# Optimization experiments

Measured on AMD Instinct MI355X. Metric: run time of the kernel, lower is better.

The kernel has to match this reference:

```python
import jax, jax.numpy as jnp
from jax import lax
import numpy as np

NPOINT, RADIUS, NSAMPLE = 1024, 0.2, 32
MLP = [64, 64, 128]
IN_CH = 35  # 3 coord channels + 32 point features
EPS = 1e-5


def farthest_point_sample(xyz, npoint):
    # xyz: (B, N, 3) -> (B, npoint) int32. Deterministic start at index 0.
    B, N, _ = xyz.shape

    def step(carry, _):
        dist, farthest = carry  # (B,N), (B,)
        centroid = jnp.take_along_axis(xyz, farthest[:, None, None], axis=1)  # (B,1,3)
        d = jnp.sum((xyz - centroid) ** 2, axis=-1)  # (B,N)
        dist = jnp.minimum(dist, d)
        nxt = jnp.argmax(dist, axis=-1).astype(jnp.int32)
        return (dist, nxt), farthest

    init = (jnp.full((B, N), 1e10, xyz.dtype), jnp.zeros((B,), jnp.int32))
    _, idxs = lax.scan(step, init, None, length=npoint)
    return idxs.T  # (B, npoint)


def gather_points(points, idx):
    # points: (B, N, C); idx: (B, ...) int -> (B, ..., C)
    return jax.vmap(lambda p, i: p[i])(points, idx)


def query_ball_point(radius, nsample, xyz, new_xyz):
    # xyz: (B,N,3), new_xyz: (B,S,3) -> (B,S,nsample) int32
    B, N, _ = xyz.shape
    sqrdists = jnp.sum((new_xyz[:, :, None, :] - xyz[:, None, :, :]) ** 2, axis=-1)  # (B,S,N)
    group_idx = jnp.where(sqrdists > radius ** 2, N, jnp.arange(N, dtype=jnp.int32))
    group_idx = jnp.sort(group_idx, axis=-1)[:, :, :nsample]
    first = group_idx[:, :, :1]
    return jnp.where(group_idx == N, first, group_idx)


def sa_forward(xyz, points, params):
    B, N, C = xyz.shape
    fps_idx = farthest_point_sample(xyz, NPOINT)
    new_xyz = gather_points(xyz, fps_idx)  # (B,S,3)
    idx = query_ball_point(RADIUS, NSAMPLE, xyz, new_xyz)  # (B,S,K)
    grouped_xyz = gather_points(xyz, idx)  # (B,S,K,3)
    grouped_xyz_norm = grouped_xyz - new_xyz[:, :, None, :]
    grouped_points = gather_points(points, idx)  # (B,S,K,D)
    new_points = jnp.concatenate([grouped_xyz_norm, grouped_points], axis=-1)  # (B,S,K,Cin)
    x = new_points.transpose(0, 3, 2, 1)  # (B, Cin, K, S)
    for w, b, g, be in params:
        x = jnp.einsum('oi,biks->boks', w, x) + b[None, :, None, None]  # 1x1 conv
        mean = x.mean(axis=(0, 2, 3), keepdims=True)  # BatchNorm2d, training mode
        var = x.var(axis=(0, 2, 3), keepdims=True)
        x = (x - mean) / jnp.sqrt(var + EPS)
        x = jax.nn.relu(g[None, :, None, None] * x + be[None, :, None, None])
    new_points_out = x.max(axis=2)  # max over nsample -> (B, Cout, S)
    return new_xyz, new_points_out


def setup_inputs() -> dict:
    key = jax.random.key(0)
    ks = jax.random.split(key, 16)
    B, N, D = 16, 4096, 32
    inp = {
        'xyz': jax.random.uniform(ks[0], (B, N, 3), dtype=jnp.float32),
        'points': jax.random.normal(ks[1], (B, N, D), dtype=jnp.float32),
    }
    last = IN_CH
    for li, out_ch in enumerate(MLP):
        inp[f'w{li}'] = jax.random.normal(ks[2 + 4 * li], (out_ch, last), dtype=jnp.float32) * 0.05
        inp[f'b{li}'] = jnp.zeros((out_ch,), jnp.float32)
        inp[f'g{li}'] = jnp.ones((out_ch,), jnp.float32)
        inp[f'be{li}'] = jnp.zeros((out_ch,), jnp.float32)
        last = out_ch
    return inp


def reference(xyz, points, w0, b0, g0, be0, w1, b1, g1, be1, w2, b2, g2, be2):
    params = [(w0, b0, g0, be0), (w1, b1, g1, be1), (w2, b2, g2, be2)]
    return sa_forward(xyz, points, params)
```

## Files before the change

kernel.cpp:

```cpp
#include <hip/hip_runtime.h>
#include <stdint.h>

#define BATCH   16
#define NPTS    4096
#define NPOINT  1024
#define NSAMPLE 32
#define NPOS    (BATCH*NPOINT*NSAMPLE)
#define EPSV    1e-5f

typedef unsigned short ushort_t;
typedef unsigned int uint_t;
typedef unsigned long long u64;
typedef __attribute__((ext_vector_type(8))) short bf16x8;
typedef __attribute__((ext_vector_type(4))) float f32x4;

__device__ inline ushort_t f2bf(float f) {
    uint_t u = __float_as_uint(f);
    u += 0x7fffu + ((u >> 16) & 1u);
    return (ushort_t)(u >> 16);
}
__device__ inline void unpack8(uint4 u, float* f) {
    f[0] = __uint_as_float(u.x << 16); f[1] = __uint_as_float(u.x & 0xffff0000u);
    f[2] = __uint_as_float(u.y << 16); f[3] = __uint_as_float(u.y & 0xffff0000u);
    f[4] = __uint_as_float(u.z << 16); f[5] = __uint_as_float(u.z & 0xffff0000u);
    f[6] = __uint_as_float(u.w << 16); f[7] = __uint_as_float(u.w & 0xffff0000u);
}
__device__ inline uint4 pack8(const float* a) {
    uint4 r;
    r.x = (uint_t)f2bf(a[0]) | ((uint_t)f2bf(a[1]) << 16);
    r.y = (uint_t)f2bf(a[2]) | ((uint_t)f2bf(a[3]) << 16);
    r.z = (uint_t)f2bf(a[4]) | ((uint_t)f2bf(a[5]) << 16);
    r.w = (uint_t)f2bf(a[6]) | ((uint_t)f2bf(a[7]) << 16);
    return r;
}

__global__ void zero_kernel(float* __restrict__ p, int n) {
    int i = blockIdx.x * blockDim.x + threadIdx.x;
    if (i < n) p[i] = 0.f;
}

#define DPP_MAX_STAGE(CTRL) do {                                              \
    uint_t _lo2 = __builtin_amdgcn_update_dpp(lo, lo, CTRL, 0xf, 0xf, false); \
    uint_t _hi2 = __builtin_amdgcn_update_dpp(hi, hi, CTRL, 0xf, 0xf, false); \
    u64 _o = ((u64)_hi2 << 32) | _lo2;                                        \
    u64 _v = ((u64)hi << 32) | lo;                                            \
    bool _g = _o > _v;                                                        \
    lo = _g ? _lo2 : lo; hi = _g ? _hi2 : hi;                                 \
} while (0)

__global__ __launch_bounds__(256) void fps_kernel(const float* __restrict__ xyz,
                                                  float* __restrict__ new_xyz) {
    __shared__ float4 lxyz[NPTS];
    __shared__ u64 wbest[2][4];
    __shared__ int fpsidx[NPOINT];
    const int b = blockIdx.x;
    const int tid = threadIdx.x;
    const float* base = xyz + (size_t)b * NPTS * 3;
    for (int n = tid; n < NPTS; n += 256) {
        lxyz[n] = make_float4(base[3 * n], base[3 * n + 1], base[3 * n + 2], 0.f);
    }
    __syncthreads();

    float px[16], py[16], pz[16], dist[16];
    uint_t lowc[16];
#pragma unroll
    for (int j = 0; j < 16; j++) {
        float4 v = lxyz[tid + j * 256];
        px[j] = v.x; py[j] = v.y; pz[j] = v.z;
        dist[j] = 1e10f;
        lowc[j] = ~(uint_t)(tid + j * 256);
    }
    if (tid == 0) fpsidx[0] = 0;
    int cur = 0;
    const int lane = tid & 63, wid = tid >> 6;

    for (int it = 1; it < NPOINT; ++it) {
        float4 c = lxyz[cur];
#pragma unroll
        for (int j = 0; j < 16; j++) {
            float dx = __fsub_rn(px[j], c.x);
            float dy = __fsub_rn(py[j], c.y);
            float dz = __fsub_rn(pz[j], c.z);
            float d = __fadd_rn(__fadd_rn(__fmul_rn(dx, dx), __fmul_rn(dy, dy)),
                                __fmul_rn(dz, dz));
            dist[j] = fminf(dist[j], d);
        }
        u64 t[8];
#pragma unroll
        for (int j = 0; j < 8; j++) {
            u64 a = ((u64)__float_as_uint(dist[j]) << 32) | lowc[j];
            u64 d2 = ((u64)__float_as_uint(dist[j + 8]) << 32) | lowc[j + 8];
            t[j] = a > d2 ? a : d2;
        }
#pragma unroll
        for (int j = 0; j < 4; j++) { u64 o = t[j + 4]; t[j] = t[j] > o ? t[j] : o; }
        t[0] = t[0] > t[1] ? t[0] : t[1];
        t[2] = t[2] > t[3] ? t[2] : t[3];
        u64 v = t[0] > t[2] ? t[0] : t[2];

        uint_t lo = (uint_t)v, hi = (uint_t)(v >> 32);
        DPP_MAX_STAGE(0x111);
        DPP_MAX_STAGE(0x112);
        DPP_MAX_STAGE(0x114);
        DPP_MAX_STAGE(0x118);
        DPP_MAX_STAGE(0x142);
        DPP_MAX_STAGE(0x143);
        uint_t mlo = __builtin_amdgcn_readlane(lo, 63);
        uint_t mhi = __builtin_amdgcn_readlane(hi, 63);

        const int par = it & 1;
        if (lane == 0) wbest[par][wid] = ((u64)mhi << 32) | mlo;
        __syncthreads();
        u64 b0 = wbest[par][0], b1 = wbest[par][1];
        u64 b2 = wbest[par][2], b3 = wbest[par][3];
        u64 m01 = b0 > b1 ? b0 : b1;
        u64 m23 = b2 > b3 ? b2 : b3;
        u64 bb = m01 > m23 ? m01 : m23;
        cur = (int)(~(uint_t)bb) & (NPTS - 1);
        if (tid == 0) fpsidx[it] = cur;
    }
    __syncthreads();
    float* ob = new_xyz + (size_t)b * NPOINT * 3;
    for (int s = tid; s < NPOINT; s += 256) {
        float4 v = lxyz[fpsidx[s]];
        ob[3 * s + 0] = v.x; ob[3 * s + 1] = v.y; ob[3 * s + 2] = v.z;
    }
}

__global__ __launch_bounds__(256) void ballq_kernel(const float* __restrict__ xyz,
                                                    const float* __restrict__ new_xyz,
                                                    int* __restrict__ gidx) {
    const int gw = (int)((blockIdx.x * 256 + threadIdx.x) >> 6);
    const int lane = threadIdx.x & 63;
    const int b = gw / NPOINT, s = gw % NPOINT;
    const float* nb = new_xyz + ((size_t)b * NPOINT + s) * 3;
    const float cx = nb[0], cy = nb[1], cz = nb[2];
    const float* xb = xyz + (size_t)b * NPTS * 3;
    const float r2 = (float)(0.2 * 0.2);
    int cnt = 0;
    int first = -1;
    int* out = gidx + (size_t)gw * NSAMPLE;
    for (int j0 = 0; j0 < NPTS; j0 += 64) {
        int j = j0 + lane;
        float dx = __fsub_rn(xb[j * 3 + 0], cx);
        float dy = __fsub_rn(xb[j * 3 + 1], cy);
        float dz = __fsub_rn(xb[j * 3 + 2], cz);
        float d = __fadd_rn(__fadd_rn(__fmul_rn(dx, dx), __fmul_rn(dy, dy)),
                            __fmul_rn(dz, dz));
        bool pred = !(d > r2);
        u64 mask = __ballot(pred);
        if (first < 0 && mask != 0ull) first = j0 + (__ffsll((long long)mask) - 1);
        int before = __popcll(mask & ((1ull << lane) - 1ull));
        int slot = cnt + before;
        if (pred && slot < NSAMPLE) out[slot] = j;
        cnt += (int)__popcll(mask);
        if (cnt >= NSAMPLE) break;
    }
    if (cnt < NSAMPLE) {
        if (lane >= cnt && lane < NSAMPLE) out[lane] = first;
    }
}

__global__ __launch_bounds__(256) void conv1_mfma(const float* __restrict__ xyz,
                                                  const float* __restrict__ points,
                                                  const float* __restrict__ new_xyz,
                                                  const int* __restrict__ gidx,
                                                  const float* __restrict__ W,
                                                  const float* __restrict__ bias,
                                                  ushort_t* __restrict__ Y) {
    const int lane = threadIdx.x & 63, wid = threadIdx.x >> 6;
    const int l15 = lane & 15, quad = lane >> 4;
    const int p0 = blockIdx.x * 128 + wid * 32;

    bf16x8 Bp[4], Bx[4];
#pragma unroll
    for (int nt = 0; nt < 4; nt++) {
        const float* wr = W + (size_t)(nt * 16 + l15) * 35;
#pragma unroll
        for (int q = 0; q < 8; q++) Bp[nt][q] = (short)f2bf(wr[3 + quad * 8 + q]);
#pragma unroll
        for (int q = 0; q < 8; q++)
            Bx[nt][q] = (quad == 0 && q < 3) ? (short)f2bf(wr[q]) : (short)0;
    }
    f32x4 acc[2][4];
#pragma unroll
    for (int mt = 0; mt < 2; mt++)
#pragma unroll
        for (int nt = 0; nt < 4; nt++) acc[mt][nt] = (f32x4){0.f, 0.f, 0.f, 0.f};

#pragma unroll
    for (int mt = 0; mt < 2; mt++) {
        const int p = p0 + mt * 16 + l15;
        const int b = p >> 15, s = (p & 32767) >> 5;
        const int j = gidx[p];
        const float* pr = points + ((size_t)(b * NPTS + j)) * 32 + quad * 8;
        bf16x8 Ap, Ax;
#pragma unroll
        for (int q = 0; q < 8; q++) Ap[q] = (short)f2bf(pr[q]);
#pragma unroll
        for (int q = 0; q < 8; q++) Ax[q] = 0;
        const float* xp = xyz + ((size_t)(b * NPTS + j)) * 3;
        const float* nz = new_xyz + ((size_t)(b * NPOINT + s)) * 3;
        if (quad == 0) {
            Ax[0] = (short)f2bf(xp[0] - nz[0]);
            Ax[1] = (short)f2bf(xp[1] - nz[1]);
            Ax[2] = (short)f2bf(xp[2] - nz[2]);
        }
#pragma unroll
        for (int nt = 0; nt < 4; nt++) {
            acc[mt][nt] = __builtin_amdgcn_mfma_f32_16x16x32_bf16(Ap, Bp[nt], acc[mt][nt], 0, 0, 0);
            acc[mt][nt] = __builtin_amdgcn_mfma_f32_16x16x32_bf16(Ax, Bx[nt], acc[mt][nt], 0, 0, 0);
        }
    }
#pragma unroll
    for (int nt = 0; nt < 4; nt++) {
        const int ch = nt * 16 + l15;
        const float bs = bias[ch];
#pragma unroll
        for (int mt = 0; mt < 2; mt++) {
            const int pb = p0 + mt * 16 + quad * 4;
#pragma unroll
            for (int r = 0; r < 4; r++)
                Y[(size_t)(pb + r) * 64 + ch] = f2bf(acc[mt][nt][r] + bs);
        }
    }
}

template <int IN, int OUT>
__global__ __launch_bounds__(256) void convN_mfma(const ushort_t* __restrict__ Yin,
                                                  const float* __restrict__ scale,
                                                  const float* __restrict__ shift,
                                                  const float* __restrict__ W,
                                                  const float* __restrict__ bias,
                                                  ushort_t* __restrict__ Yout) {
    constexpr int NT = OUT / 16;
    const int lane = threadIdx.x & 63, wid = threadIdx.x >> 6;
    const int l15 = lane & 15, quad = lane >> 4;
    const int p0 = blockIdx.x * 128 + wid * 32;

    float sc[2][8], sh[2][8];
#pragma unroll
    for (int kq = 0; kq < 2; kq++) {
        const int i0 = kq * 32 + quad * 8;
#pragma unroll
        for (int q = 0; q < 8; q++) { sc[kq][q] = scale[i0 + q]; sh[kq][q] = shift[i0 + q]; }
    }
    bf16x8 Bf[NT][2];
#pragma unroll
    for (int nt = 0; nt < NT; nt++)
#pragma unroll
        for (int kq = 0; kq < 2; kq++) {
            const float* wr = W + (size_t)(nt * 16 + l15) * IN + kq * 32 + quad * 8;
#pragma unroll
            for (int q = 0; q < 8; q++) Bf[nt][kq][q] = (short)f2bf(wr[q]);
        }

    bf16x8 Af[2][2];
#pragma unroll
    for (int mt = 0; mt < 2; mt++)
#pragma unroll
        for (int kq = 0; kq < 2; kq++) {
            const ushort_t* yr = Yin + (size_t)(p0 + mt * 16 + l15) * IN + kq * 32 + quad * 8;
            uint4 u = *(const uint4*)yr;
            float f[8]; unpack8(u, f);
#pragma unroll
            for (int q = 0; q < 8; q++) {
                float x = fmaxf(fmaf(f[q], sc[kq][q], sh[kq][q]), 0.f);
                Af[mt][kq][q] = (short)f2bf(x);
            }
        }

    f32x4 acc[2][NT];
#pragma unroll
    for (int mt = 0; mt < 2; mt++)
#pragma unroll
        for (int nt = 0; nt < NT; nt++) acc[mt][nt] = (f32x4){0.f, 0.f, 0.f, 0.f};
#pragma unroll
    for (int mt = 0; mt < 2; mt++)
#pragma unroll
        for (int nt = 0; nt < NT; nt++) {
            acc[mt][nt] = __builtin_amdgcn_mfma_f32_16x16x32_bf16(Af[mt][0], Bf[nt][0], acc[mt][nt], 0, 0, 0);
            acc[mt][nt] = __builtin_amdgcn_mfma_f32_16x16x32_bf16(Af[mt][1], Bf[nt][1], acc[mt][nt], 0, 0, 0);
        }
#pragma unroll
    for (int nt = 0; nt < NT; nt++) {
        const int ch = nt * 16 + l15;
        const float bs = bias[ch];
#pragma unroll
        for (int mt = 0; mt < 2; mt++) {
            const int pb = p0 + mt * 16 + quad * 4;
#pragma unroll
            for (int r = 0; r < 4; r++)
                Yout[(size_t)(pb + r) * OUT + ch] = f2bf(acc[mt][nt][r] + bs);
        }
    }
}

template <int OUT>
__global__ __launch_bounds__(256) void stats_kernel(const ushort_t* __restrict__ Y,
                                                    float* __restrict__ sums,
                                                    float* __restrict__ sq) {
    constexpr int CH8 = OUT / 8;
    constexpr int ROWS = 256 / CH8;
    constexpr int PPB = ROWS * 32;
    const int oc = threadIdx.x % CH8;
    const int row = threadIdx.x / CH8;
    const int p0 = blockIdx.x * PPB + row;
    float s[8], q[8];
#pragma unroll
    for (int i = 0; i < 8; i++) { s[i] = 0.f; q[i] = 0.f; }
    for (int jj = 0; jj < 32; jj++) {
        int p = p0 + jj * ROWS;
        uint4 u = *(const uint4*)(Y + (size_t)p * OUT + oc * 8);
        float f[8];
        unpack8(u, f);
#pragma unroll
        for (int i = 0; i < 8; i++) { s[i] += f[i]; q[i] += f[i] * f[i]; }
    }
#pragma unroll
    for (int m = CH8; m < 64; m <<= 1) {
#pragma unroll
        for (int i = 0; i < 8; i++) {
            s[i] += __shfl_xor(s[i], m, 64);
            q[i] += __shfl_xor(q[i], m, 64);
        }
    }
    __shared__ float lsq[4][CH8][16];
    const int wid = threadIdx.x >> 6, lane = threadIdx.x & 63;
    if (lane < CH8) {
#pragma unroll
        for (int i = 0; i < 8; i++) {
            lsq[wid][lane][i] = s[i];
            lsq[wid][lane][8 + i] = q[i];
        }
    }
    __syncthreads();
    if (threadIdx.x < OUT) {
        int ch = threadIdx.x;
        int oc2 = ch >> 3, i = ch & 7;
        float ssum = 0.f, qsum = 0.f;
#pragma unroll
        for (int w = 0; w < 4; w++) {
            ssum += lsq[w][oc2][i];
            qsum += lsq[w][oc2][8 + i];
        }
        atomicAdd(sums + ch, ssum);
        atomicAdd(sq + ch, qsum);
    }
}

__global__ void finalize_kernel(const float* __restrict__ sums, const float* __restrict__ sq,
                                const float* __restrict__ g, const float* __restrict__ be,
                                float* __restrict__ scale, float* __restrict__ shift, int OUT) {
    int c = threadIdx.x;
    if (c < OUT) {
        float mean = sums[c] * (1.f / (float)NPOS);
        float var = sq[c] * (1.f / (float)NPOS) - mean * mean;
        float inv = 1.f / sqrtf(var + EPSV);
        float sc = g[c] * inv;
        scale[c] = sc;
        shift[c] = be[c] - mean * sc;
    }
}

__global__ __launch_bounds__(256) void final_kernel(const ushort_t* __restrict__ Y3,
                                                    const float* __restrict__ scale,
                                                    const float* __restrict__ shift,
                                                    float* __restrict__ out) {
    const int b = blockIdx.x >> 5;
    const int stile = (blockIdx.x & 31) * 32;
    const int sl = threadIdx.x >> 3;
    const int oc = threadIdx.x & 7;
    const int s = stile + sl;
    const size_t base = ((size_t)(b * NPOINT + s)) * 32 * 128 + oc * 16;
    float vmax[16];
#pragma unroll
    for (int i = 0; i < 16; i++) vmax[i] = 0.f;
    for (int k = 0; k < 32; k++) {
        const ushort_t* yp = Y3 + base + (size_t)k * 128;
#pragma unroll
        for (int h = 0; h < 2; h++) {
            uint4 u = *(const uint4*)(yp + h * 8);
            float f[8];
            unpack8(u, f);
#pragma unroll
            for (int i = 0; i < 8; i++) {
                int o = oc * 16 + h * 8 + i;
                float v = fmaf(f[i], scale[o], shift[o]);
                vmax[h * 8 + i] = fmaxf(vmax[h * 8 + i], v);
            }
        }
    }
    __shared__ float res[32][130];
#pragma unroll
    for (int i = 0; i < 16; i++) res[sl][oc * 16 + i] = vmax[i];
    __syncthreads();
    const int so = threadIdx.x & 31;
    const int og = threadIdx.x >> 5;
#pragma unroll
    for (int r = 0; r < 16; r++) {
        int o = og * 16 + r;
        out[((size_t)(b * 128 + o)) * NPOINT + stile + so] = res[so][o];
    }
}

extern "C" void kernel_launch(void* const* d_in, const int* in_sizes, int n_in,
                              void* d_out, int out_size, void* d_ws, size_t ws_size,
                              hipStream_t stream) {
    const float* xyz = (const float*)d_in[0];
    const float* points = (const float*)d_in[1];
    const float* w0 = (const float*)d_in[2];
    const float* b0 = (const float*)d_in[3];
    const float* g0 = (const float*)d_in[4];
    const float* be0 = (const float*)d_in[5];
    const float* w1 = (const float*)d_in[6];
    const float* b1 = (const float*)d_in[7];
    const float* g1 = (const float*)d_in[8];
    const float* be1 = (const float*)d_in[9];
    const float* w2 = (const float*)d_in[10];
    const float* b2 = (const float*)d_in[11];
    const float* g2 = (const float*)d_in[12];
    const float* be2 = (const float*)d_in[13];

    float* out = (float*)d_out;
    float* new_xyz = out;
    float* final_out = out + BATCH * NPOINT * 3;

    char* ws = (char*)d_ws;
    const size_t MB = 1024u * 1024u;
    const size_t o_gidx = 0;
    const size_t o_y2 = 2 * MB;
    const size_t o_y13 = o_y2 + (size_t)NPOS * 64 * 2;
    const size_t o_stats = o_y13 + (size_t)NPOS * 128 * 2;
    const size_t o_params = o_stats + 2048;

    int* gidx = (int*)(ws + o_gidx);
    ushort_t* Y1 = (ushort_t*)(ws + o_y13);
    ushort_t* Y2 = (ushort_t*)(ws + o_y2);
    ushort_t* Y3 = (ushort_t*)(ws + o_y13);
    float* st = (float*)(ws + o_stats);
    float* sum1 = st + 0, *sq1 = st + 64;
    float* sum2 = st + 128, *sq2 = st + 192;
    float* sum3 = st + 256, *sq3 = st + 384;
    float* pr = (float*)(ws + o_params);
    float* scale1 = pr + 0, *shift1 = pr + 64;
    float* scale2 = pr + 128, *shift2 = pr + 192;
    float* scale3 = pr + 256, *shift3 = pr + 384;

    zero_kernel<<<1, 512, 0, stream>>>(st, 512);

    fps_kernel<<<BATCH, 256, 0, stream>>>(xyz, new_xyz);
    ballq_kernel<<<(BATCH * NPOINT) / 4, 256, 0, stream>>>(xyz, new_xyz, gidx);
    conv1_mfma<<<NPOS / 128, 256, 0, stream>>>(xyz, points, new_xyz, gidx, w0, b0, Y1);
    stats_kernel<64><<<NPOS / 1024, 256, 0, stream>>>(Y1, sum1, sq1);
    finalize_kernel<<<1, 128, 0, stream>>>(sum1, sq1, g0, be0, scale1, shift1, 64);
    convN_mfma<64, 64><<<NPOS / 128, 256, 0, stream>>>(Y1, scale1, shift1, w1, b1, Y2);
    stats_kernel<64><<<NPOS / 1024, 256, 0, stream>>>(Y2, sum2, sq2);
    finalize_kernel<<<1, 128, 0, stream>>>(sum2, sq2, g1, be1, scale2, shift2, 64);
    convN_mfma<64, 128><<<NPOS / 128, 256, 0, stream>>>(Y2, scale2, shift2, w2, b2, Y3);
    stats_kernel<128><<<NPOS / 512, 256, 0, stream>>>(Y3, sum3, sq3);
    finalize_kernel<<<1, 128, 0, stream>>>(sum3, sq3, g2, be2, scale3, shift3, 128);
    final_kernel<<<BATCH * 32, 256, 0, stream>>>(Y3, scale3, shift3, final_out);
}
```

Baseline: 1.076 ms.

## Fuse BatchNorm statistics into conv epilogues and pack FPS math as float2

Removes the three separate stats kernels. Each conv kernel now accumulates per-channel sum and sum-of-squares of its bf16-rounded outputs in the epilogue, reduces them across lanes and waves, and issues atomics, so the activations are not re-read from memory. Separately, the FPS distance update is rewritten with two-wide float vectors to allow packed FP32 math, with fp contraction disabled to keep rounding exact. The cost is more atomics (one set per 128-point block instead of per 512 or 1024) and extra epilogue work and LDS in the conv kernels.

```diff
diff --git a/kernel.cpp b/kernel.cpp
--- a/kernel.cpp
+++ b/kernel.cpp
@@ -1,5 +1,7 @@
 #include <hip/hip_runtime.h>
 #include <stdint.h>
+
+#pragma clang fp contract(off)
 
 #define BATCH   16
 #define NPTS    4096
@@ -13,6 +15,7 @@
 typedef unsigned long long u64;
 typedef __attribute__((ext_vector_type(8))) short bf16x8;
 typedef __attribute__((ext_vector_type(4))) float f32x4;
+typedef __attribute__((ext_vector_type(2))) float f32x2;
 
 __device__ inline ushort_t f2bf(float f) {
     uint_t u = __float_as_uint(f);
@@ -24,14 +27,6 @@
     f[2] = __uint_as_float(u.y << 16); f[3] = __uint_as_float(u.y & 0xffff0000u);
     f[4] = __uint_as_float(u.z << 16); f[5] = __uint_as_float(u.z & 0xffff0000u);
     f[6] = __uint_as_float(u.w << 16); f[7] = __uint_as_float(u.w & 0xffff0000u);
-}
-__device__ inline uint4 pack8(const float* a) {
-    uint4 r;
-    r.x = (uint_t)f2bf(a[0]) | ((uint_t)f2bf(a[1]) << 16);
-    r.y = (uint_t)f2bf(a[2]) | ((uint_t)f2bf(a[3]) << 16);
-    r.z = (uint_t)f2bf(a[4]) | ((uint_t)f2bf(a[5]) << 16);
-    r.w = (uint_t)f2bf(a[6]) | ((uint_t)f2bf(a[7]) << 16);
-    return r;
 }
 
 __global__ void zero_kernel(float* __restrict__ p, int n) {
@@ -61,14 +56,18 @@
     }
     __syncthreads();
 
-    float px[16], py[16], pz[16], dist[16];
+    f32x2 px[8], py[8], pz[8], dist[8];
     uint_t lowc[16];
 #pragma unroll
-    for (int j = 0; j < 16; j++) {
-        float4 v = lxyz[tid + j * 256];
-        px[j] = v.x; py[j] = v.y; pz[j] = v.z;
-        dist[j] = 1e10f;
-        lowc[j] = ~(uint_t)(tid + j * 256);
+    for (int j = 0; j < 8; j++) {
+        float4 v0 = lxyz[tid + (2 * j) * 256];
+        float4 v1 = lxyz[tid + (2 * j + 1) * 256];
+        px[j] = (f32x2){v0.x, v1.x};
+        py[j] = (f32x2){v0.y, v1.y};
+        pz[j] = (f32x2){v0.z, v1.z};
+        dist[j] = (f32x2){1e10f, 1e10f};
+        lowc[2 * j] = ~(uint_t)(tid + (2 * j) * 256);
+        lowc[2 * j + 1] = ~(uint_t)(tid + (2 * j + 1) * 256);
     }
     if (tid == 0) fpsidx[0] = 0;
     int cur = 0;
@@ -76,21 +75,21 @@
 
     for (int it = 1; it < NPOINT; ++it) {
         float4 c = lxyz[cur];
-#pragma unroll
-        for (int j = 0; j < 16; j++) {
-            float dx = __fsub_rn(px[j], c.x);
-            float dy = __fsub_rn(py[j], c.y);
-            float dz = __fsub_rn(pz[j], c.z);
-            float d = __fadd_rn(__fadd_rn(__fmul_rn(dx, dx), __fmul_rn(dy, dy)),
-                                __fmul_rn(dz, dz));
-            dist[j] = fminf(dist[j], d);
-        }
+        const f32x2 cx = (f32x2){c.x, c.x};
+        const f32x2 cy = (f32x2){c.y, c.y};
+        const f32x2 cz = (f32x2){c.z, c.z};
         u64 t[8];
 #pragma unroll
         for (int j = 0; j < 8; j++) {
-            u64 a = ((u64)__float_as_uint(dist[j]) << 32) | lowc[j];
-            u64 d2 = ((u64)__float_as_uint(dist[j + 8]) << 32) | lowc[j + 8];
-            t[j] = a > d2 ? a : d2;
+            f32x2 dx = px[j] - cx;
+            f32x2 dy = py[j] - cy;
+            f32x2 dz = pz[j] - cz;
+            f32x2 d = (dx * dx + dy * dy) + dz * dz;
+            f32x2 nd = __builtin_elementwise_min(dist[j], d);
+            dist[j] = nd;
+            u64 e0 = ((u64)__float_as_uint(nd.x) << 32) | lowc[2 * j];
+            u64 e1 = ((u64)__float_as_uint(nd.y) << 32) | lowc[2 * j + 1];
+            t[j] = e0 > e1 ? e0 : e1;
         }
 #pragma unroll
         for (int j = 0; j < 4; j++) { u64 o = t[j + 4]; t[j] = t[j] > o ? t[j] : o; }
@@ -167,7 +166,9 @@
                                                   const int* __restrict__ gidx,
                                                   const float* __restrict__ W,
                                                   const float* __restrict__ bias,
-                                                  ushort_t* __restrict__ Y) {
+                                                  ushort_t* __restrict__ Y,
+                                                  float* __restrict__ sums,
+                                                  float* __restrict__ sq) {
     const int lane = threadIdx.x & 63, wid = threadIdx.x >> 6;
     const int l15 = lane & 15, quad = lane >> 4;
     const int p0 = blockIdx.x * 128 + wid * 32;
@@ -212,6 +213,9 @@
             acc[mt][nt] = __builtin_amdgcn_mfma_f32_16x16x32_bf16(Ax, Bx[nt], acc[mt][nt], 0, 0, 0);
         }
     }
+    float s_[4], q_[4];
+#pragma unroll
+    for (int nt = 0; nt < 4; nt++) { s_[nt] = 0.f; q_[nt] = 0.f; }
 #pragma unroll
     for (int nt = 0; nt < 4; nt++) {
         const int ch = nt * 16 + l15;
@@ -220,8 +224,35 @@
         for (int mt = 0; mt < 2; mt++) {
             const int pb = p0 + mt * 16 + quad * 4;
 #pragma unroll
-            for (int r = 0; r < 4; r++)
-                Y[(size_t)(pb + r) * 64 + ch] = f2bf(acc[mt][nt][r] + bs);
+            for (int r = 0; r < 4; r++) {
+                float x = acc[mt][nt][r] + bs;
+                uint_t u = __float_as_uint(x);
+                u += 0x7fffu + ((u >> 16) & 1u);
+                Y[(size_t)(pb + r) * 64 + ch] = (ushort_t)(u >> 16);
+                float v = __uint_as_float(u & 0xffff0000u);
+                s_[nt] += v; q_[nt] += v * v;
+            }
+        }
+    }
+#pragma unroll
+    for (int nt = 0; nt < 4; nt++) {
+        s_[nt] += __shfl_xor(s_[nt], 16, 64); s_[nt] += __shfl_xor(s_[nt], 32, 64);
+        q_[nt] += __shfl_xor(q_[nt], 16, 64); q_[nt] += __shfl_xor(q_[nt], 32, 64);
+    }
+    __shared__ float reds[4][4][16], redq[4][4][16];
+    if (lane < 16) {
+#pragma unroll
+        for (int nt = 0; nt < 4; nt++) { reds[wid][nt][lane] = s_[nt]; redq[wid][nt][lane] = q_[nt]; }
+    }
+    __syncthreads();
+    if (threadIdx.x < 16) {
+#pragma unroll
+        for (int nt = 0; nt < 4; nt++) {
+            float ss = 0.f, qq = 0.f;
+#pragma unroll
+            for (int w = 0; w < 4; w++) { ss += reds[w][nt][threadIdx.x]; qq += redq[w][nt][threadIdx.x]; }
+            atomicAdd(sums + nt * 16 + threadIdx.x, ss);
+            atomicAdd(sq + nt * 16 + threadIdx.x, qq);
         }
     }
 }
@@ -232,7 +263,9 @@
                                                   const float* __restrict__ shift,
                                                   const float* __restrict__ W,
                                                   const float* __restrict__ bias,
-                                                  ushort_t* __restrict__ Yout) {
+                                                  ushort_t* __restrict__ Yout,
+                                                  float* __restrict__ sums,
+                                                  float* __restrict__ sq) {
     constexpr int NT = OUT / 16;
     const int lane = threadIdx.x & 63, wid = threadIdx.x >> 6;
     const int l15 = lane & 15, quad = lane >> 4;
@@ -282,6 +315,9 @@
             acc[mt][nt] = __builtin_amdgcn_mfma_f32_16x16x32_bf16(Af[mt][0], Bf[nt][0], acc[mt][nt], 0, 0, 0);
             acc[mt][nt] = __builtin_amdgcn_mfma_f32_16x16x32_bf16(Af[mt][1], Bf[nt][1], acc[mt][nt], 0, 0, 0);
         }
+    float s_[NT], q_[NT];
+#pragma unroll
+    for (int nt = 0; nt < NT; nt++) { s_[nt] = 0.f; q_[nt] = 0.f; }
 #pragma unroll
     for (int nt = 0; nt < NT; nt++) {
         const int ch = nt * 16 + l15;
@@ -290,62 +326,36 @@
         for (int mt = 0; mt < 2; mt++) {
             const int pb = p0 + mt * 16 + quad * 4;
 #pragma unroll
-            for (int r = 0; r < 4; r++)
-                Yout[(size_t)(pb + r) * OUT + ch] = f2bf(acc[mt][nt][r] + bs);
-        }
-    }
-}
-
-template <int OUT>
-__global__ __launch_bounds__(256) void stats_kernel(const ushort_t* __restrict__ Y,
-                                                    float* __restrict__ sums,
-                                                    float* __restrict__ sq) {
-    constexpr int CH8 = OUT / 8;
-    constexpr int ROWS = 256 / CH8;
-    constexpr int PPB = ROWS * 32;
-    const int oc = threadIdx.x % CH8;
-    const int row = threadIdx.x / CH8;
-    const int p0 = blockIdx.x * PPB + row;
-    float s[8], q[8];
-#pragma unroll
-    for (int i = 0; i < 8; i++) { s[i] = 0.f; q[i] = 0.f; }
-    for (int jj = 0; jj < 32; jj++) {
-        int p = p0 + jj * ROWS;
-        uint4 u = *(const uint4*)(Y + (size_t)p * OUT + oc * 8);
-        float f[8];
-        unpack8(u, f);
-#pragma unroll
-        for (int i = 0; i < 8; i++) { s[i] += f[i]; q[i] += f[i] * f[i]; }
-    }
-#pragma unroll
-    for (int m = CH8; m < 64; m <<= 1) {
-#pragma unroll
-        for (int i = 0; i < 8; i++) {
-            s[i] += __shfl_xor(s[i], m, 64);
-            q[i] += __shfl_xor(q[i], m, 64);
-        }
-    }
-    __shared__ float lsq[4][CH8][16];
-    const int wid = threadIdx.x >> 6, lane = threadIdx.x & 63;
-    if (lane < CH8) {
-#pragma unroll
-        for (int i = 0; i < 8; i++) {
-            lsq[wid][lane][i] = s[i];
-            lsq[wid][lane][8 + i] = q[i];
-        }
+            for (int r = 0; r < 4; r++) {
+                float x = acc[mt][nt][r] + bs;
+                uint_t u = __float_as_uint(x);
+                u += 0x7fffu + ((u >> 16) & 1u);
+                Yout[(size_t)(pb + r) * OUT + ch] = (ushort_t)(u >> 16);
+                float v = __uint_as_float(u & 0xffff0000u);
+                s_[nt] += v; q_[nt] += v * v;
+            }
+        }
+    }
+#pragma unroll
+    for (int nt = 0; nt < NT; nt++) {
+        s_[nt] += __shfl_xor(s_[nt], 16, 64); s_[nt] += __shfl_xor(s_[nt], 32, 64);
+        q_[nt] += __shfl_xor(q_[nt], 16, 64); q_[nt] += __shfl_xor(q_[nt], 32, 64);
+    }
+    __shared__ float reds[4][NT][16], redq[4][NT][16];
+    if (lane < 16) {
+#pragma unroll
+        for (int nt = 0; nt < NT; nt++) { reds[wid][nt][lane] = s_[nt]; redq[wid][nt][lane] = q_[nt]; }
     }
     __syncthreads();
-    if (threadIdx.x < OUT) {
-        int ch = threadIdx.x;
-        int oc2 = ch >> 3, i = ch & 7;
-        float ssum = 0.f, qsum = 0.f;
-#pragma unroll
-        for (int w = 0; w < 4; w++) {
-            ssum += lsq[w][oc2][i];
-            qsum += lsq[w][oc2][8 + i];
-        }
-        atomicAdd(sums + ch, ssum);
-        atomicAdd(sq + ch, qsum);
+    if (threadIdx.x < 16) {
+#pragma unroll
+        for (int nt = 0; nt < NT; nt++) {
+            float ss = 0.f, qq = 0.f;
+#pragma unroll
+            for (int w = 0; w < 4; w++) { ss += reds[w][nt][threadIdx.x]; qq += redq[w][nt][threadIdx.x]; }
+            atomicAdd(sums + nt * 16 + threadIdx.x, ss);
+            atomicAdd(sq + nt * 16 + threadIdx.x, qq);
+        }
     }
 }
 
@@ -451,14 +461,11 @@
 
     fps_kernel<<<BATCH, 256, 0, stream>>>(xyz, new_xyz);
     ballq_kernel<<<(BATCH * NPOINT) / 4, 256, 0, stream>>>(xyz, new_xyz, gidx);
-    conv1_mfma<<<NPOS / 128, 256, 0, stream>>>(xyz, points, new_xyz, gidx, w0, b0, Y1);
-    stats_kernel<64><<<NPOS / 1024, 256, 0, stream>>>(Y1, sum1, sq1);
+    conv1_mfma<<<NPOS / 128, 256, 0, stream>>>(xyz, points, new_xyz, gidx, w0, b0, Y1, sum1, sq1);
     finalize_kernel<<<1, 128, 0, stream>>>(sum1, sq1, g0, be0, scale1, shift1, 64);
-    convN_mfma<64, 64><<<NPOS / 128, 256, 0, stream>>>(Y1, scale1, shift1, w1, b1, Y2);
-    stats_kernel<64><<<NPOS / 1024, 256, 0, stream>>>(Y2, sum2, sq2);
+    convN_mfma<64, 64><<<NPOS / 128, 256, 0, stream>>>(Y1, scale1, shift1, w1, b1, Y2, sum2, sq2);
     finalize_kernel<<<1, 128, 0, stream>>>(sum2, sq2, g1, be1, scale2, shift2, 64);
-    convN_mfma<64, 128><<<NPOS / 128, 256, 0, stream>>>(Y2, scale2, shift2, w2, b2, Y3);
-    stats_kernel<128><<<NPOS / 512, 256, 0, stream>>>(Y3, sum3, sq3);
+    convN_mfma<64, 128><<<NPOS / 128, 256, 0, stream>>>(Y2, scale2, shift2, w2, b2, Y3, sum3, sq3);
     finalize_kernel<<<1, 128, 0, stream>>>(sum3, sq3, g2, be2, scale3, shift3, 128);
     final_kernel<<<BATCH * 32, 256, 0, stream>>>(Y3, scale3, shift3, final_out);
 }
```

Measured after the change: 1.113 ms. 3.5% more time.
